# Kernel optimization log

Hardware: AMD Instinct MI355X
Metric: run time of the kernel (lower is better)

## Reference

```python
import jax, jax.numpy as jnp
import numpy as np

N_SRC = 50000; N_DST = 50000; E = 800000
IN_NODE = 128; IN_EDGE = 16; OUT_NODE = 64; OUT_EDGE = 16; H = 4
LEAKY_SLOPE = 0.01  # F.leaky_relu default used inside dgl EGATConv


def setup_inputs() -> dict:
    key = jax.random.key(0)
    ks = jax.random.split(key, 11)
    return dict(
        nfeats=jax.random.normal(ks[0], (N_SRC, IN_NODE), jnp.float32),
        dst_feats=jax.random.normal(ks[1], (N_DST, IN_NODE), jnp.float32),
        reward=jax.random.uniform(ks[2], (E,), jnp.float32),
        src=jax.random.randint(ks[3], (E,), 0, N_SRC),
        dst=jax.random.randint(ks[4], (E,), 0, N_DST),
        W_ns=jax.random.normal(ks[5], (IN_NODE, H * OUT_NODE), jnp.float32) * 0.05,
        b_ns=jnp.zeros((H * OUT_NODE,), jnp.float32),
        W_ni=jax.random.normal(ks[6], (IN_NODE, H * OUT_EDGE), jnp.float32) * 0.05,
        W_nj=jax.random.normal(ks[7], (IN_NODE, H * OUT_EDGE), jnp.float32) * 0.05,
        W_fij=jax.random.normal(ks[8], (IN_EDGE, H * OUT_EDGE), jnp.float32) * 0.05,
        attn=jax.random.normal(ks[9], (H, OUT_EDGE), jnp.float32) * 0.05,
        b_e=jnp.zeros((H * OUT_EDGE,), jnp.float32),
    )


def reference(nfeats, dst_feats, reward, src, dst,
              W_ns, b_ns, W_ni, W_nj, W_fij, attn, b_e):
    # EGAT.forward with num_layers=1: efeats = reward repeated to IN_EDGE cols
    efeats = jnp.repeat(reward[:, None], IN_EDGE, axis=1)              # (E, Fe_in)
    # --- EGATConv ---
    f_ni = nfeats @ W_ni                                               # (Ns, H*Fe)
    f_nj = dst_feats @ W_nj                                            # (Nd, H*Fe)
    f_out = f_ni[src] + f_nj[dst] + efeats @ W_fij + b_e               # (E, H*Fe)
    f_out = jax.nn.leaky_relu(f_out, LEAKY_SLOPE).reshape(E, H, OUT_EDGE)
    e = jnp.einsum('ehf,hf->eh', f_out, attn)                          # (E, H)
    # edge softmax over incoming edges of each dst node (stable)
    m = jax.ops.segment_max(e, dst, num_segments=N_DST)                # (Nd, H)
    a = jnp.exp(e - m[dst])
    s = jax.ops.segment_sum(a, dst, num_segments=N_DST)                # (Nd, H)
    a = a / jnp.where(s > 0, s, 1.0)[dst]                              # (E, H)
    # weighted aggregation of projected src features
    h_src = (nfeats @ W_ns + b_ns).reshape(N_SRC, H, OUT_NODE)
    msg = h_src[src] * a[:, :, None]                                   # (E, H, Fn)
    h_out = jax.ops.segment_sum(msg, dst, num_segments=N_DST)          # (Nd, H, Fn)
    # wrapper: mean over heads then ReLU
    return jax.nn.relu(h_out.mean(axis=1))                             # (Nd, Fn)
```

## Files before the change

### kernel.cpp

```cpp
#include <hip/hip_runtime.h>

#define IN_NODE 128
#define OUT_NODE 64
#define NHEAD 4
#define HN 256
#define HE 64
#define LEAKY 0.01f
#define MAXD 96

typedef __attribute__((ext_vector_type(8))) short bf16x8;
typedef __attribute__((ext_vector_type(4))) float f32x4;

__device__ __forceinline__ float bf2f(unsigned short u) {
    union { unsigned u; float f; } v; v.u = ((unsigned)u) << 16; return v.f;
}
__device__ __forceinline__ unsigned short f2bf(float x) {
    union { float f; unsigned u; } v; v.f = x;
    unsigned r = v.u + 0x7FFF + ((v.u >> 16) & 1);
    return (unsigned short)(r >> 16);
}
__device__ __forceinline__ bf16x8 cvt8(float4 a, float4 b) {
    bf16x8 r;
    r[0] = (short)f2bf(a.x); r[1] = (short)f2bf(a.y);
    r[2] = (short)f2bf(a.z); r[3] = (short)f2bf(a.w);
    r[4] = (short)f2bf(b.x); r[5] = (short)f2bf(b.y);
    r[6] = (short)f2bf(b.z); r[7] = (short)f2bf(b.w);
    return r;
}

__global__ void prep_hist(const float* __restrict__ W_fij,
                          const float* __restrict__ W_ni,
                          const float* __restrict__ W_ns,
                          const float* __restrict__ W_nj,
                          const int* __restrict__ dst,
                          float* __restrict__ wsum, unsigned short* __restrict__ WT,
                          int* __restrict__ cnt, int E) {
    int b = blockIdx.x;
    if (b == 0) {
        int k = threadIdx.x;
        if (k < 64) {
            float s = 0.f;
#pragma unroll
            for (int c = 0; c < 16; ++c) s += W_fij[c * 64 + k];
            wsum[k] = s;
        }
        return;
    }
    if (b <= 12) {
        int base = (b - 1) * 4096 + threadIdx.x;
#pragma unroll
        for (int i = 0; i < 16; ++i) {
            int idx = base + i * 256;
            unsigned short v;
            if (idx < 8192)      { int n = idx >> 7, k = idx & 127; v = f2bf(W_ni[k * 64 + n]); }
            else if (idx < 40960){ int j = idx - 8192;  int n = j >> 7, k = j & 127; v = f2bf(W_ns[k * 256 + n]); }
            else                 { int j = idx - 40960; int n = j >> 7, k = j & 127; v = f2bf(W_nj[k * 64 + n]); }
            WT[idx] = v;
        }
        return;
    }
    int i = (b - 13) * 256 + threadIdx.x;
    if (i < E) atomicAdd(&cnt[dst[i]], 1);
}

__global__ __launch_bounds__(256) void scan_all(const int* __restrict__ cnt,
                                                int* __restrict__ row_ptr,
                                                int* __restrict__ partials,
                                                int* __restrict__ flags,
                                                int n, int E, int nb) {
    __shared__ int sums[256];
    __shared__ int s_base;
    int tid = threadIdx.x, b = blockIdx.x;
    int base = b * 1024;
    int v[4]; int tsum = 0;
#pragma unroll
    for (int j = 0; j < 4; ++j) {
        int idx = base + tid * 4 + j;
        v[j] = (idx < n) ? cnt[idx] : 0;
        tsum += v[j];
    }
    sums[tid] = tsum;
    __syncthreads();
    for (int off = 1; off < 256; off <<= 1) {
        int x = (tid >= off) ? sums[tid - off] : 0;
        __syncthreads();
        sums[tid] += x;
        __syncthreads();
    }
    if (tid == 255) {
        __hip_atomic_store(&partials[b], sums[255], __ATOMIC_RELAXED, __HIP_MEMORY_SCOPE_AGENT);
        __hip_atomic_store(&flags[b], 1, __ATOMIC_RELEASE, __HIP_MEMORY_SCOPE_AGENT);
    }
    if (tid < 64) {
        int val = 0;
        if (tid < nb) {
            while (__hip_atomic_load(&flags[tid], __ATOMIC_ACQUIRE, __HIP_MEMORY_SCOPE_AGENT) == 0) {
                __builtin_amdgcn_s_sleep(1);
            }
            val = __hip_atomic_load(&partials[tid], __ATOMIC_RELAXED, __HIP_MEMORY_SCOPE_AGENT);
        }
#pragma unroll
        for (int o = 1; o < 64; o <<= 1) {
            int x = __shfl_up(val, o);
            if (tid >= o) val += x;
        }
        int off = (b > 0) ? __shfl(val, b - 1) : 0;
        if (tid == 0) s_base = off;
    }
    __syncthreads();
    int run = s_base + sums[tid] - tsum;
#pragma unroll
    for (int j = 0; j < 4; ++j) {
        int idx = base + tid * 4 + j;
        if (idx < n) row_ptr[idx] = run;
        run += v[j];
    }
    if (b == nb - 1 && tid == 0) row_ptr[n] = E;
}

__global__ __launch_bounds__(256) void mega(
    const float* __restrict__ nfeats, const float* __restrict__ dst_feats,
    const unsigned short* __restrict__ WT, const float* __restrict__ b_ns,
    const int* __restrict__ src, const int* __restrict__ dst,
    const float* __restrict__ reward, const int* __restrict__ row_ptr,
    int* __restrict__ cnt,
    unsigned short* __restrict__ f_ni, unsigned short* __restrict__ h_src,
    unsigned short* __restrict__ f_nj, int2* __restrict__ sr_s,
    int Ns, int Nd, int E, int nG, int nScatter)
{
    const int g = blockIdx.x / 5, r = blockIdx.x % 5;
    if (r < 3) {
        const int gb = g * 3 + r;
        if (gb >= nG) return;
        const int gy = gb % 6;
        const int bx = gb / 6;
        const float* A; const unsigned short* wt; const float* bias = nullptr;
        unsigned short* C; int M, N, colBase;
        if (gy == 0)      { A = nfeats;    wt = WT;         C = f_ni;  M = Ns; N = 64;  colBase = 0; }
        else if (gy <= 4) { A = nfeats;    wt = WT + 8192;  C = h_src; M = Ns; N = 256; colBase = (gy - 1) * 64; bias = b_ns; }
        else              { A = dst_feats; wt = WT + 40960; C = f_nj;  M = Nd; N = 64;  colBase = 0; }

        const int w = threadIdx.x >> 6, lane = threadIdx.x & 63;
        const int rowW = bx * 64 + w * 16;
        if (rowW >= M) return;
        const int m = lane & 15, q = lane >> 4;
        int lrow = rowW + m; if (lrow >= M) lrow = M - 1;
        const float* arow = A + (size_t)lrow * 128 + q * 8;

        f32x4 acc0 = {}, acc1 = {}, acc2 = {}, acc3 = {};
#pragma unroll
        for (int kc = 0; kc < 128; kc += 32) {
            float4 a0 = *reinterpret_cast<const float4*>(arow + kc);
            float4 a1 = *reinterpret_cast<const float4*>(arow + kc + 4);
            bf16x8 af = cvt8(a0, a1);
            const unsigned short* bp = wt + (size_t)(colBase + m) * 128 + kc + q * 8;
            bf16x8 b0 = *reinterpret_cast<const bf16x8*>(bp);
            bf16x8 b1 = *reinterpret_cast<const bf16x8*>(bp + 16 * 128);
            bf16x8 b2 = *reinterpret_cast<const bf16x8*>(bp + 32 * 128);
            bf16x8 b3 = *reinterpret_cast<const bf16x8*>(bp + 48 * 128);
            acc0 = __builtin_amdgcn_mfma_f32_16x16x32_bf16(af, b0, acc0, 0, 0, 0);
            acc1 = __builtin_amdgcn_mfma_f32_16x16x32_bf16(af, b1, acc1, 0, 0, 0);
            acc2 = __builtin_amdgcn_mfma_f32_16x16x32_bf16(af, b2, acc2, 0, 0, 0);
            acc3 = __builtin_amdgcn_mfma_f32_16x16x32_bf16(af, b3, acc3, 0, 0, 0);
        }

#pragma unroll
        for (int f = 0; f < 4; ++f) {
            f32x4 a = (f == 0) ? acc0 : (f == 1) ? acc1 : (f == 2) ? acc2 : acc3;
            int col = colBase + f * 16 + m;
            float bv = bias ? bias[col] : 0.f;
#pragma unroll
            for (int rr = 0; rr < 4; ++rr) {
                int orow = rowW + q * 4 + rr;
                if (orow < M) C[(size_t)orow * N + col] = f2bf(a[rr] + bv);
            }
        }
        return;
    }
    const int sb = g * 2 + (r - 3);
    if (sb >= nScatter) return;
    int i = sb * 256 + threadIdx.x;
    if (i >= E) return;
    int d = dst[i];
    int pos = row_ptr[d] + atomicSub(&cnt[d], 1) - 1;
    sr_s[pos] = make_int2(src[i], __float_as_int(reward[i]));
}

__global__ __launch_bounds__(256) void fused_agg(
    const unsigned short* __restrict__ f_ni, const unsigned short* __restrict__ f_nj,
    const unsigned short* __restrict__ h_src, const int2* __restrict__ sr_s,
    const int* __restrict__ row_ptr,
    const float* __restrict__ wsum, const float* __restrict__ b_e,
    const float* __restrict__ attn, float* __restrict__ out, int Nd)
{
    __shared__ float s_e[4][MAXD][4];
    __shared__ int   s_sn[4][MAXD];
    const int wv = threadIdx.x >> 6, lane = threadIdx.x & 63;
    const int d = blockIdx.x * 4 + wv;
    if (d >= Nd) return;
    const int l = lane & 15, sub = lane >> 4;
    const int beg = row_ptr[d];
    const int end = row_ptr[d + 1];

    for (int i = lane; i < MAXD; i += 64) s_sn[wv][i] = -1;

    ushort4 uj = *reinterpret_cast<const ushort4*>(f_nj + (size_t)d * HE + 4 * l);
    float4 fnj = { bf2f(uj.x), bf2f(uj.y), bf2f(uj.z), bf2f(uj.w) };
    float4 ws = *reinterpret_cast<const float4*>(wsum + 4 * l);
    float4 be = *reinterpret_cast<const float4*>(b_e + 4 * l);
    float4 at = *reinterpret_cast<const float4*>(attn + 4 * l);

    float den = 0.f;
    for (int base = beg; base < end; base += 4) {
        int slot = base + sub;
        if (slot < end) {
            int2 sr = sr_s[slot];
            int sn = sr.x;
            float r = __int_as_float(sr.y);
            ushort4 ui = *reinterpret_cast<const ushort4*>(f_ni + (size_t)sn * HE + 4 * l);
            float t, v;
            v = bf2f(ui.x) + fnj.x + r * ws.x + be.x; v = (v >= 0.f) ? v : LEAKY * v; t  = v * at.x;
            v = bf2f(ui.y) + fnj.y + r * ws.y + be.y; v = (v >= 0.f) ? v : LEAKY * v; t += v * at.y;
            v = bf2f(ui.z) + fnj.z + r * ws.z + be.z; v = (v >= 0.f) ? v : LEAKY * v; t += v * at.z;
            v = bf2f(ui.w) + fnj.w + r * ws.w + be.w; v = (v >= 0.f) ? v : LEAKY * v; t += v * at.w;
            t += __shfl_xor(t, 1);
            t += __shfl_xor(t, 2);
            float ev = __expf(t);
            den += ev;
            int idx = slot - beg;
            if (idx < MAXD) {
                if ((l & 3) == 0) s_e[wv][idx][l >> 2] = ev;
                if (l == 0) s_sn[wv][idx] = sn;
            }
        }
    }
    den += __shfl_xor(den, 16);
    den += __shfl_xor(den, 32);
    float dh = __shfl(den, (lane >> 4) << 2);
    float invh = (dh > 0.f) ? 1.f / dh : 0.f;
    const int h = lane >> 4;

    float a0 = 0.f, a1 = 0.f, a2 = 0.f, a3 = 0.f;
    int cap = min(end - beg, MAXD);
    int npad = (cap + 7) & ~7;
    for (int idx0 = 0; idx0 < npad; idx0 += 8) {
#pragma unroll
        for (int j = 0; j < 8; ++j) {
            int idx = idx0 + j;
            int sn = s_sn[wv][idx];
            float wgt = (sn >= 0) ? s_e[wv][idx][h] * invh : 0.f;
            int sa = (sn >= 0) ? sn : 0;
            ushort4 u = *reinterpret_cast<const ushort4*>(h_src + (size_t)sa * HN + lane * 4);
            a0 = fmaf(wgt, bf2f(u.x), a0);
            a1 = fmaf(wgt, bf2f(u.y), a1);
            a2 = fmaf(wgt, bf2f(u.z), a2);
            a3 = fmaf(wgt, bf2f(u.w), a3);
        }
    }
    for (int slot = beg + MAXD; slot < end; ++slot) {
        int2 sr = sr_s[slot];
        int sn = sr.x;
        float r = __int_as_float(sr.y);
        float v = bf2f(f_ni[(size_t)sn * HE + lane]) + bf2f(f_nj[(size_t)d * HE + lane])
                + r * wsum[lane] + b_e[lane];
        v = (v >= 0.f) ? v : LEAKY * v;
        float t = v * attn[lane];
        t += __shfl_xor(t, 1);
        t += __shfl_xor(t, 2);
        t += __shfl_xor(t, 4);
        t += __shfl_xor(t, 8);
        float wgt = __expf(t) * invh;
        ushort4 u = *reinterpret_cast<const ushort4*>(h_src + (size_t)sn * HN + lane * 4);
        a0 = fmaf(wgt, bf2f(u.x), a0);
        a1 = fmaf(wgt, bf2f(u.y), a1);
        a2 = fmaf(wgt, bf2f(u.z), a2);
        a3 = fmaf(wgt, bf2f(u.w), a3);
    }

    a0 += __shfl_xor(a0, 16); a0 += __shfl_xor(a0, 32);
    a1 += __shfl_xor(a1, 16); a1 += __shfl_xor(a1, 32);
    a2 += __shfl_xor(a2, 16); a2 += __shfl_xor(a2, 32);
    a3 += __shfl_xor(a3, 16); a3 += __shfl_xor(a3, 32);
    if (lane < 16) {
        float4 o = { fmaxf(a0 * 0.25f, 0.f), fmaxf(a1 * 0.25f, 0.f),
                     fmaxf(a2 * 0.25f, 0.f), fmaxf(a3 * 0.25f, 0.f) };
        *reinterpret_cast<float4*>(out + (size_t)d * OUT_NODE + lane * 4) = o;
    }
}

static inline char* align256(char* p) {
    return (char*)(((uintptr_t)p + 255) & ~(uintptr_t)255);
}

extern "C" void kernel_launch(void* const* d_in, const int* in_sizes, int n_in,
                              void* d_out, int out_size, void* d_ws, size_t ws_size,
                              hipStream_t stream) {
    const float* nfeats    = (const float*)d_in[0];
    const float* dst_feats = (const float*)d_in[1];
    const float* reward    = (const float*)d_in[2];
    const int*   src       = (const int*)d_in[3];
    const int*   dst       = (const int*)d_in[4];
    const float* W_ns      = (const float*)d_in[5];
    const float* b_ns      = (const float*)d_in[6];
    const float* W_ni      = (const float*)d_in[7];
    const float* W_nj      = (const float*)d_in[8];
    const float* W_fij     = (const float*)d_in[9];
    const float* attn      = (const float*)d_in[10];
    const float* b_e       = (const float*)d_in[11];
    float* out = (float*)d_out;

    const int Ns = in_sizes[0] / IN_NODE;
    const int Nd = in_sizes[1] / IN_NODE;
    const int E  = in_sizes[2];

    char* ws = (char*)d_ws;
    unsigned short* f_ni  = (unsigned short*)ws; ws = align256(ws + (size_t)Ns * HE * 2);
    unsigned short* f_nj  = (unsigned short*)ws; ws = align256(ws + (size_t)Nd * HE * 2);
    unsigned short* h_src = (unsigned short*)ws; ws = align256(ws + (size_t)Ns * HN * 2);
    unsigned short* WT    = (unsigned short*)ws; ws = align256(ws + 49152 * 2);
    float* wsum    = (float*)ws; ws = align256(ws + HE * 4);
    int*   cnt     = (int*)ws;
    int*   flags   = cnt + Nd;   ws = align256(ws + (size_t)(Nd + 64) * 4);
    int*   row_ptr = (int*)ws;   ws = align256(ws + (size_t)(Nd + 1) * 4);
    int*   partials= (int*)ws;   ws = align256(ws + 256 * 4);
    int2*  sr_s    = (int2*)ws;  ws = align256(ws + (size_t)E * 8);

    hipMemsetAsync(cnt, 0, (size_t)(Nd + 64) * 4, stream);

    prep_hist<<<13 + (E + 255) / 256, 256, 0, stream>>>(
        W_fij, W_ni, W_ns, W_nj, dst, wsum, WT, cnt, E);

    int nb = (Nd + 1023) / 1024;
    scan_all<<<nb, 256, 0, stream>>>(cnt, row_ptr, partials, flags, Nd, E, nb);

    int Mmax = (Ns > Nd) ? Ns : Nd;
    int nG = ((Mmax + 63) / 64) * 6;
    int nScatter = (E + 255) / 256;
    int nGroups = ((nG + 2) / 3 > (nScatter + 1) / 2) ? (nG + 2) / 3 : (nScatter + 1) / 2;
    mega<<<nGroups * 5, 256, 0, stream>>>(
        nfeats, dst_feats, WT, b_ns, src, dst, reward, row_ptr, cnt,
        f_ni, h_src, f_nj, sr_s, Ns, Nd, E, nG, nScatter);

    fused_agg<<<(Nd + 3) / 4, 256, 0, stream>>>(
        f_ni, f_nj, h_src, sr_s, row_ptr, wsum, b_e, attn, out, Nd);
}
```

Before: 315.4 us.

## Stage A tile in LDS once and compute all weight columns per block

The GEMM part of the mega kernel now loads each 64-row input tile once into swizzled shared memory as bf16. One block then computes all 20 column groups for nfeats (f_ni and h_src) or 4 for dst_feats. Before, the same rows were reloaded from global memory for each of the 6 column slices. The weight transpose is also reordered into an MFMA-fragment layout so each lane reads B fragments with contiguous 16-byte loads. The cost is higher register pressure (20 accumulators), 16KB of LDS per block that lowers occupancy, and fewer, heavier GEMM blocks interleaved with the scatter blocks.

```diff
diff --git a/kernel.cpp b/kernel.cpp
--- a/kernel.cpp
+++ b/kernel.cpp
@@ -51,10 +51,17 @@
 #pragma unroll
         for (int i = 0; i < 16; ++i) {
             int idx = base + i * 256;
+            int g   = idx >> 11;
+            int rem = idx & 2047;
+            int c   = rem >> 9;
+            int l   = (rem >> 3) & 63;
+            int j   = rem & 7;
+            int nl  = l & 15;
+            int k   = c * 32 + (l >> 4) * 8 + j;
             unsigned short v;
-            if (idx < 8192)      { int n = idx >> 7, k = idx & 127; v = f2bf(W_ni[k * 64 + n]); }
-            else if (idx < 40960){ int j = idx - 8192;  int n = j >> 7, k = j & 127; v = f2bf(W_ns[k * 256 + n]); }
-            else                 { int j = idx - 40960; int n = j >> 7, k = j & 127; v = f2bf(W_nj[k * 64 + n]); }
+            if (g < 4)       v = f2bf(W_ni[k * 64  + g * 16 + nl]);
+            else if (g < 20) v = f2bf(W_ns[k * 256 + (g - 4) * 16 + nl]);
+            else             v = f2bf(W_nj[k * 64  + (g - 20) * 16 + nl]);
             WT[idx] = v;
         }
         return;
@@ -118,6 +125,66 @@
     if (b == nb - 1 && tid == 0) row_ptr[n] = E;
 }
 
+template<int NG, int G0>
+__device__ __forceinline__ void gemm_tile(
+    const float* __restrict__ A, int rowBase, int M,
+    const unsigned short* __restrict__ WB, const float* __restrict__ b_ns,
+    unsigned short* __restrict__ f_ni, unsigned short* __restrict__ h_src,
+    unsigned short* __restrict__ f_nj, unsigned short* As)
+{
+    const int t = threadIdx.x;
+    const float4* A4 = reinterpret_cast<const float4*>(A);
+#pragma unroll
+    for (int j = 0; j < 4; ++j) {
+        int gi = j * 256 + t;
+        int r  = gi >> 4;
+        int gr = rowBase + r; if (gr >= M) gr = M - 1;
+        int fi = (gi & 15) * 2;
+        float4 a0 = A4[(size_t)gr * 32 + fi];
+        float4 a1 = A4[(size_t)gr * 32 + fi + 1];
+        int byteoff = (gi * 16) ^ ((r & 7) << 4);
+        *reinterpret_cast<bf16x8*>(reinterpret_cast<char*>(As) + byteoff) = cvt8(a0, a1);
+    }
+    __syncthreads();
+
+    const int lane = t & 63, w = t >> 6;
+    const int rw = rowBase + w * 16;
+    if (rw >= M) return;
+    const int m = lane & 15, q = lane >> 4;
+    const int tr = w * 16 + m;
+
+    f32x4 acc[NG] = {};
+    const char* Asb = reinterpret_cast<const char*>(As);
+#pragma unroll
+    for (int c = 0; c < 4; ++c) {
+        int gi  = tr * 16 + c * 4 + q;
+        int off = (gi * 16) ^ ((tr & 7) << 4);
+        bf16x8 af = *reinterpret_cast<const bf16x8*>(Asb + off);
+#pragma unroll
+        for (int g = 0; g < NG; ++g) {
+            bf16x8 bf = *reinterpret_cast<const bf16x8*>(
+                WB + (size_t)(((G0 + g) * 4 + c) * 64 + lane) * 8);
+            acc[g] = __builtin_amdgcn_mfma_f32_16x16x32_bf16(af, bf, acc[g], 0, 0, 0);
+        }
+    }
+
+#pragma unroll
+    for (int g = 0; g < NG; ++g) {
+        const int ga = G0 + g;
+        unsigned short* C; int N, colBase; const float* bias = nullptr;
+        if (ga < 4)       { C = f_ni;  N = 64;  colBase = ga * 16; }
+        else if (ga < 20) { C = h_src; N = 256; colBase = (ga - 4) * 16; bias = b_ns; }
+        else              { C = f_nj;  N = 64;  colBase = (ga - 20) * 16; }
+        int col = colBase + m;
+        float bv = bias ? bias[col] : 0.f;
+#pragma unroll
+        for (int rr = 0; rr < 4; ++rr) {
+            int orow = rw + q * 4 + rr;
+            if (orow < M) C[(size_t)orow * N + col] = f2bf(acc[g][rr] + bv);
+        }
+    }
+}
+
 __global__ __launch_bounds__(256) void mega(
     const float* __restrict__ nfeats, const float* __restrict__ dst_feats,
     const unsigned short* __restrict__ WT, const float* __restrict__ b_ns,
@@ -126,58 +193,19 @@
     int* __restrict__ cnt,
     unsigned short* __restrict__ f_ni, unsigned short* __restrict__ h_src,
     unsigned short* __restrict__ f_nj, int2* __restrict__ sr_s,
-    int Ns, int Nd, int E, int nG, int nScatter)
+    int Ns, int Nd, int E, int nBlkNf, int nBlkDj, int nScatter)
 {
-    const int g = blockIdx.x / 5, r = blockIdx.x % 5;
-    if (r < 3) {
-        const int gb = g * 3 + r;
-        if (gb >= nG) return;
-        const int gy = gb % 6;
-        const int bx = gb / 6;
-        const float* A; const unsigned short* wt; const float* bias = nullptr;
-        unsigned short* C; int M, N, colBase;
-        if (gy == 0)      { A = nfeats;    wt = WT;         C = f_ni;  M = Ns; N = 64;  colBase = 0; }
-        else if (gy <= 4) { A = nfeats;    wt = WT + 8192;  C = h_src; M = Ns; N = 256; colBase = (gy - 1) * 64; bias = b_ns; }
-        else              { A = dst_feats; wt = WT + 40960; C = f_nj;  M = Nd; N = 64;  colBase = 0; }
-
-        const int w = threadIdx.x >> 6, lane = threadIdx.x & 63;
-        const int rowW = bx * 64 + w * 16;
-        if (rowW >= M) return;
-        const int m = lane & 15, q = lane >> 4;
-        int lrow = rowW + m; if (lrow >= M) lrow = M - 1;
-        const float* arow = A + (size_t)lrow * 128 + q * 8;
-
-        f32x4 acc0 = {}, acc1 = {}, acc2 = {}, acc3 = {};
-#pragma unroll
-        for (int kc = 0; kc < 128; kc += 32) {
-            float4 a0 = *reinterpret_cast<const float4*>(arow + kc);
-            float4 a1 = *reinterpret_cast<const float4*>(arow + kc + 4);
-            bf16x8 af = cvt8(a0, a1);
-            const unsigned short* bp = wt + (size_t)(colBase + m) * 128 + kc + q * 8;
-            bf16x8 b0 = *reinterpret_cast<const bf16x8*>(bp);
-            bf16x8 b1 = *reinterpret_cast<const bf16x8*>(bp + 16 * 128);
-            bf16x8 b2 = *reinterpret_cast<const bf16x8*>(bp + 32 * 128);
-            bf16x8 b3 = *reinterpret_cast<const bf16x8*>(bp + 48 * 128);
-            acc0 = __builtin_amdgcn_mfma_f32_16x16x32_bf16(af, b0, acc0, 0, 0, 0);
-            acc1 = __builtin_amdgcn_mfma_f32_16x16x32_bf16(af, b1, acc1, 0, 0, 0);
-            acc2 = __builtin_amdgcn_mfma_f32_16x16x32_bf16(af, b2, acc2, 0, 0, 0);
-            acc3 = __builtin_amdgcn_mfma_f32_16x16x32_bf16(af, b3, acc3, 0, 0, 0);
-        }
-
-#pragma unroll
-        for (int f = 0; f < 4; ++f) {
-            f32x4 a = (f == 0) ? acc0 : (f == 1) ? acc1 : (f == 2) ? acc2 : acc3;
-            int col = colBase + f * 16 + m;
-            float bv = bias ? bias[col] : 0.f;
-#pragma unroll
-            for (int rr = 0; rr < 4; ++rr) {
-                int orow = rowW + q * 4 + rr;
-                if (orow < M) C[(size_t)orow * N + col] = f2bf(a[rr] + bv);
-            }
+    __shared__ __align__(16) unsigned short As[64 * 128];
+    const int g = blockIdx.x / 3, r = blockIdx.x % 3;
+    if (r == 0) {
+        if (g < nBlkNf) {
+            gemm_tile<20, 0>(nfeats, g * 64, Ns, WT, b_ns, f_ni, h_src, f_nj, As);
+        } else if (g < nBlkNf + nBlkDj) {
+            gemm_tile<4, 20>(dst_feats, (g - nBlkNf) * 64, Nd, WT, b_ns, f_ni, h_src, f_nj, As);
         }
         return;
     }
-    const int sb = g * 2 + (r - 3);
+    const int sb = g * 2 + (r - 1);
     if (sb >= nScatter) return;
     int i = sb * 256 + threadIdx.x;
     if (i >= E) return;
@@ -333,13 +361,14 @@
     int nb = (Nd + 1023) / 1024;
     scan_all<<<nb, 256, 0, stream>>>(cnt, row_ptr, partials, flags, Nd, E, nb);
 
-    int Mmax = (Ns > Nd) ? Ns : Nd;
-    int nG = ((Mmax + 63) / 64) * 6;
+    int nBlkNf = (Ns + 63) / 64;
+    int nBlkDj = (Nd + 63) / 64;
+    int nG = nBlkNf + nBlkDj;
     int nScatter = (E + 255) / 256;
-    int nGroups = ((nG + 2) / 3 > (nScatter + 1) / 2) ? (nG + 2) / 3 : (nScatter + 1) / 2;
-    mega<<<nGroups * 5, 256, 0, stream>>>(
+    int nGroups = (nG > (nScatter + 1) / 2) ? nG : (nScatter + 1) / 2;
+    mega<<<nGroups * 3, 256, 0, stream>>>(
         nfeats, dst_feats, WT, b_ns, src, dst, reward, row_ptr, cnt,
-        f_ni, h_src, f_nj, sr_s, Ns, Nd, E, nG, nScatter);
+        f_ni, h_src, f_nj, sr_s, Ns, Nd, E, nBlkNf, nBlkDj, nScatter);
 
     fused_agg<<<(Nd + 3) / 4, 256, 0, stream>>>(
         f_ni, f_nj, h_src, sr_s, row_ptr, wsum, b_e, attn, out, Nd);
```

Result: faster. 282.7 us (-10.4%).
